# Optimization experiments

Measured on AMD Instinct MI355X. Metric: run time of the kernel, lower is better.

Reference implementation:

```python
import jax, jax.numpy as jnp
import numpy as np

B, P, H, W = 8, 128, 32, 32
NC = 4                 # num_classes = NUM_REL_GROUP + 1
DOBJ = 4424            # 2*DOBJ = 8848
CIN = 256
C = 128 + 8848         # 8976 GCN channel dim


def setup_inputs() -> dict:
    key = jax.random.key(0)
    ks = jax.random.split(key, 24)
    s = 0.02  # weight scale to keep activations moderate
    inp = {
        "x": jax.random.normal(ks[0], (B, CIN, H, W), jnp.float32),
        "rel_pair_idxs": jax.random.randint(ks[1], (B, P, 2), 0, 640, dtype=jnp.int32),
        "obj_rep": jax.random.normal(ks[2], (640, DOBJ), jnp.float32),
        # ADD_GCN params
        "fc_w": jax.random.normal(ks[3], (NC, CIN), jnp.float32) * s,
        "ct_w": jax.random.normal(ks[4], (128, CIN), jnp.float32) * s,
        "ct_b": jnp.zeros((128,), jnp.float32),
        # DynamicGraphConvolution params
        "A": jax.random.normal(ks[5], (NC, NC), jnp.float32) * 0.25,          # static_adj conv1d (no bias)
        "sw_w": jax.random.normal(ks[6], (C, C), jnp.float32) * s / np.sqrt(C) * 30,
        "sw_b": jnp.zeros((C,), jnp.float32),
        "cg_w": jax.random.normal(ks[7], (C, C), jnp.float32) * s / np.sqrt(C) * 30,
        "cg_b": jnp.zeros((C,), jnp.float32),
        "bn_g": jnp.ones((C,), jnp.float32),
        "bn_b": jnp.zeros((C,), jnp.float32),
        "bn_m": jnp.zeros((C,), jnp.float32),
        "bn_v": jnp.ones((C,), jnp.float32),
        "co_w": jax.random.normal(ks[8], (NC, 2 * C), jnp.float32) * s / np.sqrt(C) * 30,
        "co_b": jnp.zeros((NC,), jnp.float32),
        "dw_w": jax.random.normal(ks[9], (C, C), jnp.float32) * s / np.sqrt(C) * 30,
        "dw_b": jnp.zeros((C,), jnp.float32),
        "ll_w": jax.random.normal(ks[10], (NC, C), jnp.float32) * s / np.sqrt(C) * 30,
        "ll_b": jnp.zeros((NC,), jnp.float32),
        "mask_mat": jnp.eye(NC, dtype=jnp.float32),
    }
    return inp


def reference(x, rel_pair_idxs, obj_rep, fc_w, ct_w, ct_b, A, sw_w, sw_b,
              cg_w, cg_b, bn_g, bn_b, bn_m, bn_v, co_w, co_b, dw_w, dw_b,
              ll_w, ll_b, mask_mat):
    leaky = lambda t: jax.nn.leaky_relu(t, 0.2)
    b, cin, h, w = x.shape
    xr = x.reshape(b, cin, h * w)                                  # (B,256,HW)

    # forward_classification_sm: fc -> topk(1).mean == max over spatial
    y = jnp.einsum('oc,bcs->bos', fc_w, xr)                        # (B,NC,HW)
    out1 = y.max(-1)                                               # (B,NC)

    # forward_sam
    mask = jax.nn.sigmoid(y)                                       # (B,NC,HW)
    v = jnp.einsum('oc,bcs->bos', ct_w, xr) + ct_b[None, :, None]  # (B,128,HW)
    v = jnp.einsum('bcs,bns->bcn', v, mask)                        # (B,128,NC)

    # pairwise object features (gather), tiled over NC node slots
    o1 = obj_rep[rel_pair_idxs[..., 0]]                            # (B,P,DOBJ)
    o2 = obj_rep[rel_pair_idxs[..., 1]]
    pf = jnp.concatenate([o1, o2], -1)                             # (B,P,8848)
    p = pf.shape[1]
    pf = jnp.broadcast_to(pf[..., None], pf.shape + (NC,))         # (B,P,8848,NC)
    vb = jnp.broadcast_to(v[:, None], (b, p) + v.shape[1:])        # (B,P,128,NC)
    g = jnp.concatenate([pf, vb], 2).reshape(b * p, C, NC)         # (BP,C,NC)

    # --- DynamicGraphConvolution ---
    # static GCN: node-mix conv1d (no bias) + leaky, then channel 1x1 conv + leaky
    xs = leaky(jnp.einsum('nm,pcm->pcn', A, g))                    # (BP,C,NC)
    xs = leaky(jnp.einsum('oc,pcn->pon', sw_w, xs) + sw_b[None, :, None])
    hg = g + xs

    # dynamic adjacency
    glb = hg.mean(-1)                                              # (BP,C) gap
    glb = glb @ cg_w.T + cg_b                                      # conv_global (1x1)
    glb = (glb - bn_m) * jax.lax.rsqrt(bn_v + 1e-5) * bn_g + bn_b  # BN (eval)
    glb = leaky(glb)
    # conv_create_co_mat over cat([glb_expand, hg], ch) without materializing cat
    adj = jax.nn.sigmoid(
        jnp.einsum('oc,pc->po', co_w[:, :C], glb)[:, :, None]
        + jnp.einsum('oc,pcn->pon', co_w[:, C:], hg)
        + co_b[None, :, None])                                     # (BP,NC,NC)

    # dynamic GCN
    hd = leaky(jnp.einsum('pcn,pnm->pcm', hg, adj))
    z = leaky(jnp.einsum('oc,pcn->pon', dw_w, hd) + dw_b[None, :, None])  # (BP,C,NC)

    # head: last_linear + leaky, masked diagonal sum
    out2 = leaky(jnp.einsum('oc,pcn->pon', ll_w, z) + ll_b[None, :, None])  # (BP,NC,NC)
    out2 = (out2 * jax.lax.stop_gradient(mask_mat)).sum(-1)        # (BP,NC)

    o1b = jnp.broadcast_to(out1[:, None], (b, p, NC)).reshape(b * p, NC)
    return ((o1b + out2) * 0.5).reshape(b, p, NC)
```

## Files before the change

kernel.cpp:

```cpp
#include <hip/hip_runtime.h>
#include <stdint.h>

#define DEVI __device__ __forceinline__

typedef unsigned short u16;
typedef __bf16 bf16x8 __attribute__((ext_vector_type(8)));
typedef float f32x4 __attribute__((ext_vector_type(4)));
typedef u16 u16x8 __attribute__((ext_vector_type(8)));

DEVI u16 f2bf(float f){
  union { float f; unsigned u; } v; v.f = f;
  unsigned r = v.u + 0x7FFFu + ((v.u >> 16) & 1u);
  return (u16)(r >> 16);
}
DEVI float bf2f(u16 h){
  union { unsigned u; float f; } v; v.u = ((unsigned)h) << 16;
  return v.f;
}
DEVI float lky(float t){ return t > 0.f ? t : 0.2f * t; }

#define GLD16(gp, lp) __builtin_amdgcn_global_load_lds( \
    (const __attribute__((address_space(1))) void*)(gp), \
    (__attribute__((address_space(3))) void*)(lp), 16, 0, 0)

template<int EPI>
__global__ __launch_bounds__(1024, 4)
void gemmU(const u16* __restrict__ A, const u16* __restrict__ B,
           int Kp, int Nt, int SN, int Mreal, float* __restrict__ C, long long ldc,
           const float* __restrict__ bias, const float* __restrict__ scale,
           const float* __restrict__ off, const float* __restrict__ llw,
           float* __restrict__ oacc)
{
  __shared__ __align__(16) u16 As[2][16384];
  __shared__ __align__(16) u16 Bs[2][16384];
  const int t    = threadIdx.x;
  const int lane = t & 63;
  const int wid  = t >> 6;
  const int wr = wid >> 2, wc = wid & 3;
  const int l4 = lane >> 4, l15 = lane & 15;

  const int nwg = gridDim.x;
  const int xc = blockIdx.x & 7, pp = blockIdx.x >> 3;
  const int qq = nwg >> 3, rr = nwg & 7;
  const int wg = (xc < rr ? xc*(qq+1) : rr*(qq+1) + (xc-rr)*qq) + pp;
  const int strip_sz = (nwg / Nt) * SN;
  const int strip = wg / strip_sz, srem = wg % strip_sz;
  const int mt = srem / SN, nt = strip*SN + srem % SN;

  const size_t am0 = (size_t)mt*256;
  const size_t bn0 = (size_t)nt*256;

  f32x4 acc[4][4];
  #pragma unroll
  for (int i = 0; i < 4; ++i)
    #pragma unroll
    for (int j = 0; j < 4; ++j) acc[i][j] = f32x4{0.f,0.f,0.f,0.f};
  bf16x8 afr[4], bfr[4];

  const int NT = Kp >> 6;

  const int srl0 = t >> 3, ssl = t & 7;
  const u16* pA = A + (am0 + srl0)*(size_t)Kp;
  const u16* pB = B + (bn0 + srl0)*(size_t)Kp;
  const size_t rowskip = (size_t)128 * Kp;
  const int sco0 = ((ssl ^ (srl0 & 7))*8);
  const int sco1 = ((ssl ^ ((srl0+128) & 7))*8);

  int aoff[4], boff[4];
  #pragma unroll
  for (int mi = 0; mi < 4; ++mi){
    const int r = wr*64 + mi*16 + l15;
    aoff[mi] = r*64 + ((r & 7)*8);
  }
  #pragma unroll
  for (int ni = 0; ni < 4; ++ni){
    const int r = wc*64 + ni*16 + l15;
    boff[ni] = r*64 + ((r & 7)*8);
  }

  auto STAGE = [&](int kc, int buf){
    u16* la = &As[buf][0]; u16* lb = &Bs[buf][0];
    GLD16(pA + kc + sco0,           la + t*8);
    GLD16(pA + rowskip + kc + sco1, la + 8192 + t*8);
    GLD16(pB + kc + sco0,           lb + t*8);
    GLD16(pB + rowskip + kc + sco1, lb + 8192 + t*8);
  };

  STAGE(0, 0);
  asm volatile("s_waitcnt vmcnt(0)" ::: "memory");
  __builtin_amdgcn_s_barrier();

  #define GU_BODY(KT, RB_, WB_)                                              \
  {                                                                          \
    const int nx = ((KT)+1 < NT) ? (KT)+1 : NT-1;                            \
    STAGE(nx*64, WB_);                                                       \
    const u16* ab = &As[RB_][0];                                             \
    const u16* bb = &Bs[RB_][0];                                             \
    _Pragma("unroll")                                                        \
    for (int ks = 0; ks < 2; ++ks){                                          \
      const int sx = (ks*4 + l4)*8;                                          \
      _Pragma("unroll")                                                      \
      for (int mi = 0; mi < 4; ++mi)                                         \
        afr[mi] = *(const bf16x8*)&ab[aoff[mi] ^ sx];                        \
      _Pragma("unroll")                                                      \
      for (int ni = 0; ni < 4; ++ni)                                         \
        bfr[ni] = *(const bf16x8*)&bb[boff[ni] ^ sx];                        \
      __builtin_amdgcn_s_setprio(1);                                         \
      _Pragma("unroll")                                                      \
      for (int mi = 0; mi < 4; ++mi)                                         \
        _Pragma("unroll")                                                    \
        for (int ni = 0; ni < 4; ++ni)                                       \
          acc[mi][ni] = __builtin_amdgcn_mfma_f32_16x16x32_bf16(             \
              afr[mi], bfr[ni], acc[mi][ni], 0, 0, 0);                       \
      __builtin_amdgcn_s_setprio(0);                                         \
    }                                                                        \
    asm volatile("s_waitcnt vmcnt(0)" ::: "memory");                         \
    __builtin_amdgcn_s_barrier();                                            \
  }

  for (int kt = 0; kt < NT; kt += 2){
    GU_BODY(kt,   0, 1);
    GU_BODY(kt+1, 1, 0);
  }
  #undef GU_BODY

  const int ob0 = mt*256 + wr*64;
  const int nb0 = nt*256 + wc*64;

  if (EPI == 0){
    #pragma unroll
    for (int mi = 0; mi < 4; ++mi){
      const int ob = ob0 + mi*16 + l4*4;
      if (ob < Mreal){
        #pragma unroll
        for (int ni = 0; ni < 4; ++ni){
          const int n = nb0 + ni*16 + l15;
          *(f32x4*)&C[(size_t)n*ldc + ob] = acc[mi][ni];
        }
      }
    }
  } else if (EPI == 2){
    #pragma unroll
    for (int ni = 0; ni < 4; ++ni){
      const int n = nb0 + ni*16 + l15;
      float sa0=0.f, sa1=0.f, sa2=0.f, sa3=0.f;
      #pragma unroll
      for (int mi = 0; mi < 4; ++mi){
        const int ob = ob0 + mi*16 + l4*4;
        if (ob < Mreal){
          const float sc0=scale[ob],sc1=scale[ob+1],sc2=scale[ob+2],sc3=scale[ob+3];
          const float of0=off[ob],of1=off[ob+1],of2=off[ob+2],of3=off[ob+3];
          f32x4 a = acc[mi][ni];
          f32x4 vv = { lky(a[0]*sc0+of0), lky(a[1]*sc1+of1),
                       lky(a[2]*sc2+of2), lky(a[3]*sc3+of3) };
          *(f32x4*)&C[(size_t)n*ldc + ob] = vv;
          #pragma unroll
          for (int r = 0; r < 4; ++r){
            const float vr = vv[r];
            sa0 += llw[(size_t)0*17952 + ob + r] * vr;
            sa1 += llw[(size_t)1*17952 + ob + r] * vr;
            sa2 += llw[(size_t)2*17952 + ob + r] * vr;
            sa3 += llw[(size_t)3*17952 + ob + r] * vr;
          }
        }
      }
      float sv[4] = {sa0,sa1,sa2,sa3};
      #pragma unroll
      for (int a4 = 0; a4 < 4; ++a4){
        float tt = sv[a4];
        tt += __shfl_xor(tt, 16);
        tt += __shfl_xor(tt, 32);
        if (l4 == 0) atomicAdd(&oacc[n*4 + a4], tt);
      }
    }
  } else {
    #pragma unroll
    for (int ni = 0; ni < 4; ++ni){
      const int n = nb0 + ni*16 + l15;
      const int m = n & 3, q = n >> 2;
      float s = 0.f;
      #pragma unroll
      for (int mi = 0; mi < 4; ++mi){
        #pragma unroll
        for (int r = 0; r < 4; ++r){
          const int o = ob0 + mi*16 + l4*4 + r;
          if (o < Mreal){
            const float val = lky(acc[mi][ni][r] + bias[o]);
            s += llw[(size_t)m*8976 + o] * val;
          }
        }
      }
      s += __shfl_xor(s, 16);
      s += __shfl_xor(s, 32);
      if (l4 == 0) atomicAdd(&oacc[(q*4 + m)*4 + m], s);
    }
  }
}

__global__ __launch_bounds__(256)
void gemm_vpre(const u16* __restrict__ A, const u16* __restrict__ B,
               int Kp, int Nt, int Mreal, float* __restrict__ C, long long ldc,
               const float* __restrict__ bias)
{
  __shared__ __align__(16) u16 As[2][4096];
  __shared__ __align__(16) u16 Bs[2][4096];
  const int tid  = threadIdx.x;
  const int lane = tid & 63;
  const int wr   = (tid >> 6) >> 1, wc = (tid >> 6) & 1;
  const int l4   = lane >> 4, l15 = lane & 15;
  const int mt   = blockIdx.x / Nt, nt = blockIdx.x % Nt;

  const size_t arow = (size_t)(mt*128 + (tid>>2)) * Kp + (tid&3)*8;
  const size_t brow = (size_t)(nt*128 + (tid>>2)) * Kp + (tid&3)*8;
  const int    ldst = (tid>>2)*32 + (tid&3)*8;
  const size_t rowskip = (size_t)64 * Kp;

  f32x4 acc[4][4];
  #pragma unroll
  for (int i=0;i<4;i++)
    #pragma unroll
    for (int j=0;j<4;j++) acc[i][j] = f32x4{0.f,0.f,0.f,0.f};

  const int NT = Kp >> 5;
  {
    const u16* a0 = A + arow; const u16* b0 = B + brow;
    GLD16(a0,           &As[0][ldst]);
    GLD16(a0 + rowskip, &As[0][ldst + 2048]);
    GLD16(b0,           &Bs[0][ldst]);
    GLD16(b0 + rowskip, &Bs[0][ldst + 2048]);
  }
  __syncthreads();

  for (int kt=0; kt<NT; ++kt){
    const int cur = kt & 1;
    if (kt + 1 < NT){
      const u16* a0 = A + arow + (size_t)(kt+1)*32;
      const u16* b0 = B + brow + (size_t)(kt+1)*32;
      GLD16(a0,           &As[cur^1][ldst]);
      GLD16(a0 + rowskip, &As[cur^1][ldst + 2048]);
      GLD16(b0,           &Bs[cur^1][ldst]);
      GLD16(b0 + rowskip, &Bs[cur^1][ldst + 2048]);
    }
    bf16x8 af[4], bf[4];
    #pragma unroll
    for (int mi=0;mi<4;mi++)
      af[mi] = *(const bf16x8*)&As[cur][(wr*64 + mi*16 + l15)*32 + l4*8];
    #pragma unroll
    for (int ni=0;ni<4;ni++)
      bf[ni] = *(const bf16x8*)&Bs[cur][(wc*64 + ni*16 + l15)*32 + l4*8];
    #pragma unroll
    for (int mi=0;mi<4;mi++)
      #pragma unroll
      for (int ni=0;ni<4;ni++)
        acc[mi][ni] = __builtin_amdgcn_mfma_f32_16x16x32_bf16(af[mi], bf[ni], acc[mi][ni], 0, 0, 0);
    __syncthreads();
  }

  const int ob0 = mt*128 + wr*64;
  const int nb0 = nt*128 + wc*64;
  #pragma unroll
  for (int mi=0;mi<4;mi++)
    #pragma unroll
    for (int r=0;r<4;r++){
      const int o = ob0 + mi*16 + l4*4 + r;
      if (o < Mreal){
        const float bb = bias[o];
        #pragma unroll
        for (int ni=0;ni<4;ni++){
          const int n = nb0 + ni*16 + l15;
          C[(size_t)o*ldc + n] = acc[mi][ni][r] + bb;
        }
      }
    }
}

__global__ void k_cvt_pad(const float* __restrict__ src, int srows, int scols,
                          int lds_, int koff, u16* __restrict__ dst, int Kp)
{
  const int r = blockIdx.x;
  const int nch = Kp >> 3;
  for (int ch = threadIdx.x; ch < nch; ch += blockDim.x){
    const int k = ch*8;
    u16 o[8];
    if (r < srows){
      #pragma unroll
      for (int i=0;i<8;i++){
        const int kk = k + i;
        o[i] = (kk < scols) ? f2bf(src[(size_t)r*lds_ + koff + kk]) : (u16)0;
      }
    } else {
      #pragma unroll
      for (int i=0;i<8;i++) o[i] = 0;
    }
    u16x8 vv = { o[0],o[1],o[2],o[3],o[4],o[5],o[6],o[7] };
    *(u16x8*)&dst[(size_t)r*Kp + k] = vv;
  }
}

__global__ void k_cvt_sww(const float* __restrict__ src, u16* __restrict__ dst)
{
  const int r = blockIdx.x;
  const float* row = src + (size_t)r*8976;
  u16* d1 = dst + (size_t)r*4480;
  u16* d2 = dst + (size_t)(8976+r)*4480;
  for (int ch = threadIdx.x; ch < 560; ch += 256){
    const int k = ch*8;
    u16 a[8], b[8];
    #pragma unroll
    for (int i=0;i<8;i++){
      const int kk = k+i;
      a[i] = (kk < 4424) ? f2bf(row[kk])        : (u16)0;
      b[i] = (kk < 4424) ? f2bf(row[4424 + kk]) : (u16)0;
    }
    u16x8 va = { a[0],a[1],a[2],a[3],a[4],a[5],a[6],a[7] };
    u16x8 vb = { b[0],b[1],b[2],b[3],b[4],b[5],b[6],b[7] };
    *(u16x8*)&d1[k] = va;
    *(u16x8*)&d2[k] = vb;
  }
}

__global__ void k_cvt_obj(const float* __restrict__ obj, u16* __restrict__ dst)
{
  const int r = blockIdx.x;
  const int ab = (r >= 640);
  const float* src = obj + (size_t)(ab ? r-640 : r)*4424;
  for (int ch = threadIdx.x; ch < 560; ch += 256){
    const int k = ch*8;
    u16 o[8];
    #pragma unroll
    for (int i=0;i<8;i++){
      const int kk = k+i;
      float f = (kk < 4424) ? src[kk] : 0.f;
      if (ab) f = fabsf(f);
      o[i] = f2bf(f);
    }
    u16x8 vv = { o[0],o[1],o[2],o[3],o[4],o[5],o[6],o[7] };
    *(u16x8*)&dst[(size_t)r*4480 + k] = vv;
  }
}

__global__ void k_xT(const float* __restrict__ x, u16* __restrict__ xT)
{
  __shared__ float t[32][33];
  const int bid = blockIdx.x;
  const int b = bid >> 8; const int cs = (bid >> 5) & 7; const int ss = bid & 31;
  const int tx = threadIdx.x & 31, ty = threadIdx.x >> 5;
  #pragma unroll
  for (int i=0;i<4;i++){
    const int r = ty + i*8;
    t[r][tx] = x[((size_t)(b*256 + cs*32 + r))*1024 + ss*32 + tx];
  }
  __syncthreads();
  #pragma unroll
  for (int i=0;i<4;i++){
    const int r = ty + i*8;
    xT[((size_t)(b*1024 + ss*32 + r))*256 + cs*32 + tx] = f2bf(t[tx][r]);
  }
}

__global__ void k_ymask(const float* __restrict__ x, const float* __restrict__ fcw,
                        float* __restrict__ y, float* __restrict__ mask)
{
  __shared__ float fc[1024];
  const int b = blockIdx.x >> 2, st = blockIdx.x & 3;
  for (int i=threadIdx.x; i<1024; i+=256) fc[i] = fcw[i];
  __syncthreads();
  const int s = st*256 + threadIdx.x;
  float a0=0,a1=0,a2=0,a3=0;
  for (int c=0;c<256;c++){
    const float xv = x[((size_t)(b*256+c))*1024 + s];
    a0 += fc[c]*xv; a1 += fc[256+c]*xv; a2 += fc[512+c]*xv; a3 += fc[768+c]*xv;
  }
  const size_t base = (size_t)(b*4)*1024 + s;
  y[base]        = a0; mask[base]        = 1.f/(1.f+expf(-a0));
  y[base+1024]   = a1; mask[base+1024]   = 1.f/(1.f+expf(-a1));
  y[base+2048]   = a2; mask[base+2048]   = 1.f/(1.f+expf(-a2));
  y[base+3072]   = a3; mask[base+3072]   = 1.f/(1.f+expf(-a3));
}

__global__ void k_out1(const float* __restrict__ y, float* __restrict__ out1){
  const int bn = blockIdx.x;
  float m = -3.4e38f;
  for (int s=threadIdx.x; s<1024; s+=256) m = fmaxf(m, y[(size_t)bn*1024+s]);
  for (int o=32;o;o>>=1) m = fmaxf(m, __shfl_xor(m,o));
  __shared__ float red[4];
  if ((threadIdx.x&63)==0) red[threadIdx.x>>6] = m;
  __syncthreads();
  if (threadIdx.x==0) out1[bn] = fmaxf(fmaxf(red[0],red[1]),fmaxf(red[2],red[3]));
}

__global__ void k_v(const float* __restrict__ vpreT, const float* __restrict__ mask,
                    float* __restrict__ v){
  const int b = blockIdx.x >> 7, j = blockIdx.x & 127;
  float a[4]={0,0,0,0};
  for (int s=threadIdx.x; s<1024; s+=256){
    const float pv = vpreT[(size_t)j*8192 + b*1024 + s];
    #pragma unroll
    for (int m=0;m<4;m++) a[m] += pv * mask[((size_t)(b*4+m))*1024 + s];
  }
  __shared__ float red[4][5];
  #pragma unroll
  for (int m=0;m<4;m++){
    float t=a[m];
    for (int o=32;o;o>>=1) t += __shfl_xor(t,o);
    if ((threadIdx.x&63)==0) red[m][threadIdx.x>>6]=t;
  }
  __syncthreads();
  if (threadIdx.x<4)
    v[(size_t)(b*128+j)*4 + threadIdx.x] =
      red[threadIdx.x][0]+red[threadIdx.x][1]+red[threadIdx.x][2]+red[threadIdx.x][3];
}

__global__ void k_lv(const float* __restrict__ Am, const float* __restrict__ v,
                     float* __restrict__ lv){
  const int idx = blockIdx.x*256 + threadIdx.x;
  if (idx < 1024){
    #pragma unroll
    for (int n=0;n<4;n++){
      float s=0;
      #pragma unroll
      for (int m=0;m<4;m++) s += Am[n*4+m]*v[idx*4+m];
      lv[idx*4+n] = lky(s);
    }
  }
}

__global__ void k_sV(const float* __restrict__ sw, const float* __restrict__ lv,
                     float* __restrict__ sV){
  __shared__ float l[4096];
  for (int i=threadIdx.x; i<4096; i+=256) l[i]=lv[i];
  __syncthreads();
  const int o = blockIdx.x*256 + threadIdx.x;
  if (o >= 8976) return;
  float acc[8][4] = {};
  const float* row = sw + (size_t)o*8976 + 8848;
  for (int j=0;j<128;j++){
    const float wv = row[j];
    #pragma unroll
    for (int b=0;b<8;b++){
      const float* lb = &l[(b*128+j)*4];
      #pragma unroll
      for (int n=0;n<4;n++) acc[b][n] += wv*lb[n];
    }
  }
  #pragma unroll
  for (int b=0;b<8;b++){
    f32x4 vv = {acc[b][0],acc[b][1],acc[b][2],acc[b][3]};
    *(f32x4*)&sV[((size_t)b*8976 + o)*4] = vv;
  }
}

__global__ void k_so(const float* __restrict__ cgb, const float* __restrict__ g,
                     const float* __restrict__ b2, const float* __restrict__ m,
                     const float* __restrict__ vvar, float* __restrict__ so){
  const int o = blockIdx.x*256+threadIdx.x;
  if (o<8976){
    const float sc = g[o]*rsqrtf(vvar[o]+1e-5f);
    so[o]=sc; so[8976+o] = (cgb[o]-m[o])*sc + b2[o];
  }
}

__global__ void k_glb_t2(const float* __restrict__ U, const float* __restrict__ obj,
                         const int* __restrict__ rel,
                         const float* __restrict__ sV, const float* __restrict__ swb,
                         const float* __restrict__ v, const float* __restrict__ Am,
                         const float* __restrict__ cow, u16* __restrict__ glbB,
                         float* __restrict__ t2)
{
  const int q = blockIdx.x; const int b = q >> 7;
  const int i1 = rel[q*2], i2 = rel[q*2+1];
  const float* u1  = U + (size_t)i1*17952;
  const float* u2  = U + (size_t)i2*17952 + 8976;
  const float* u1a = U + (size_t)(640+i1)*17952;
  const float* u2a = U + (size_t)(640+i2)*17952 + 8976;
  const float* o1 = obj + (size_t)i1*4424;
  const float* o2 = obj + (size_t)i2*4424;
  float rA[4], aA[4];
  #pragma unroll
  for (int n=0;n<4;n++){
    const float s = Am[n*4]+Am[n*4+1]+Am[n*4+2]+Am[n*4+3];
    rA[n]=0.6f*s; aA[n]=0.4f*fabsf(s);
  }
  float t2a[16] = {};
  for (int c = threadIdx.x; c < 9088; c += 256){
    if (c < 8976){
      const float p1 = u1[c] + u2[c];
      const float p2 = u1a[c] + u2a[c];
      const f32x4 sv = *(const f32x4*)&sV[((size_t)b*8976 + c)*4];
      const float sb = swb[c];
      const float gs = (c < 4424) ? o1[c] : (c < 8848) ? o2[c-4424] : 0.f;
      float hg[4]; float sum = 0.f;
      #pragma unroll
      for (int n=0;n<4;n++){
        const float xs2 = lky(rA[n]*p1 + aA[n]*p2 + sv[n] + sb);
        const float g = (c < 8848) ? gs : v[((size_t)b*128 + (c-8848))*4 + n];
        hg[n] = g + xs2; sum += hg[n];
      }
      glbB[(size_t)q*9088 + c] = f2bf(0.25f*sum);
      #pragma unroll
      for (int o4=0;o4<4;o4++){
        const float cw = cow[(size_t)o4*17952 + 8976 + c];
        #pragma unroll
        for (int n=0;n<4;n++) t2a[o4*4+n] += cw*hg[n];
      }
    } else {
      glbB[(size_t)q*9088 + c] = 0;
    }
  }
  __shared__ float red[16][5];
  #pragma unroll
  for (int i=0;i<16;i++){
    float t = t2a[i];
    for (int o=32;o;o>>=1) t += __shfl_xor(t,o);
    if ((threadIdx.x&63)==0) red[i][threadIdx.x>>6]=t;
  }
  __syncthreads();
  if (threadIdx.x < 16)
    t2[q*16+threadIdx.x] = red[threadIdx.x][0]+red[threadIdx.x][1]
                          +red[threadIdx.x][2]+red[threadIdx.x][3];
}

__global__ void k_hd(const float* __restrict__ U, const float* __restrict__ obj,
                     const int* __restrict__ rel,
                     const float* __restrict__ sV, const float* __restrict__ swb,
                     const float* __restrict__ v, const float* __restrict__ Am,
                     const float* __restrict__ co1acc, const float* __restrict__ t2,
                     const float* __restrict__ cob, u16* __restrict__ hdb)
{
  const int q = blockIdx.x; const int b = q>>7;
  const int i1 = rel[q*2], i2 = rel[q*2+1];
  const float* u1  = U + (size_t)i1*17952;
  const float* u2  = U + (size_t)i2*17952 + 8976;
  const float* u1a = U + (size_t)(640+i1)*17952;
  const float* u2a = U + (size_t)(640+i2)*17952 + 8976;
  const float* o1 = obj + (size_t)i1*4424;
  const float* o2 = obj + (size_t)i2*4424;
  float rA[4], aA[4];
  #pragma unroll
  for (int n=0;n<4;n++){
    const float s = Am[n*4]+Am[n*4+1]+Am[n*4+2]+Am[n*4+3];
    rA[n]=0.6f*s; aA[n]=0.4f*fabsf(s);
  }
  __shared__ float aj[16];
  if (threadIdx.x<16){
    const int a_=threadIdx.x>>2, m=threadIdx.x&3;
    const float tt = co1acc[q*4+a_] + t2[q*16 + a_*4 + m] + cob[a_];
    aj[threadIdx.x] = 1.f/(1.f+expf(-tt));
  }
  __syncthreads();
  float ajr[16];
  #pragma unroll
  for (int i=0;i<16;i++) ajr[i]=aj[i];
  for (int c=threadIdx.x; c<9088; c+=256){
    if (c<8976){
      const float p1 = u1[c] + u2[c];
      const float p2 = u1a[c] + u2a[c];
      const f32x4 sv = *(const f32x4*)&sV[((size_t)b*8976 + c)*4];
      const float sb = swb[c];
      const float gs = (c < 4424) ? o1[c] : (c < 8848) ? o2[c-4424] : 0.f;
      float hg[4];
      #pragma unroll
      for (int n=0;n<4;n++){
        const float xs2 = lky(rA[n]*p1 + aA[n]*p2 + sv[n] + sb);
        const float g = (c < 8848) ? gs : v[((size_t)b*128 + (c-8848))*4 + n];
        hg[n] = g + xs2;
      }
      #pragma unroll
      for (int m=0;m<4;m++){
        const float hv = lky(hg[0]*ajr[m] + hg[1]*ajr[4+m] + hg[2]*ajr[8+m] + hg[3]*ajr[12+m]);
        hdb[((size_t)(q*4+m))*9088 + c] = f2bf(hv);
      }
    } else {
      #pragma unroll
      for (int m=0;m<4;m++) hdb[((size_t)(q*4+m))*9088 + c] = 0;
    }
  }
}

__global__ void k_final(const float* __restrict__ o2f, const float* __restrict__ out1,
                        const float* __restrict__ llb, const float* __restrict__ mm,
                        float* __restrict__ out)
{
  const int idx = blockIdx.x*256+threadIdx.x;
  if (idx < 4096){
    const int q = idx>>2, o = idx&3, b = q>>7;
    float s=0.f;
    #pragma unroll
    for (int m=0;m<4;m++) s += lky(o2f[(q*4+o)*4+m] + llb[o]) * mm[o*4+m];
    out[idx] = 0.5f*(out1[b*4+o] + s);
  }
}

extern "C" void kernel_launch(void* const* d_in, const int* in_sizes, int n_in,
                              void* d_out, int out_size, void* d_ws, size_t ws_size,
                              hipStream_t stream)
{
  const float* x    = (const float*)d_in[0];
  const int*   rel  = (const int*)d_in[1];
  const float* obj  = (const float*)d_in[2];
  const float* fcw  = (const float*)d_in[3];
  const float* ctw  = (const float*)d_in[4];
  const float* ctb  = (const float*)d_in[5];
  const float* Am   = (const float*)d_in[6];
  const float* sww  = (const float*)d_in[7];
  const float* swb  = (const float*)d_in[8];
  const float* cgw  = (const float*)d_in[9];
  const float* cgb  = (const float*)d_in[10];
  const float* bng  = (const float*)d_in[11];
  const float* bnb  = (const float*)d_in[12];
  const float* bnm  = (const float*)d_in[13];
  const float* bnv  = (const float*)d_in[14];
  const float* cow  = (const float*)d_in[15];
  const float* cob  = (const float*)d_in[16];
  const float* dww  = (const float*)d_in[17];
  const float* dwb  = (const float*)d_in[18];
  const float* llw  = (const float*)d_in[19];
  const float* llb  = (const float*)d_in[20];
  const float* mm   = (const float*)d_in[21];
  float* out = (float*)d_out;
  (void)in_sizes; (void)n_in; (void)out_size; (void)ws_size;

  char* ws = (char*)d_ws;
  size_t off = 0;
  auto alloc = [&](size_t bytes)->char*{
    char* p = ws + off; off = (off + bytes + 255) & ~(size_t)255; return p;
  };
  u16*   Wb    = (u16*)  alloc((size_t)9216*9088*2);
  float* U     = (float*)alloc((size_t)1280*17952*4);
  u16*   glbB  = (u16*)  alloc((size_t)1024*9088*2);
  u16*   hdb   = (u16*)  alloc((size_t)4096*9088*2);
  u16*   objB  = (u16*)  alloc((size_t)1280*4480*2);
  float* glb2  = (float*)alloc((size_t)1024*8976*4);
  u16*   xT    = (u16*)  alloc((size_t)8192*256*2);
  u16*   ctwb  = (u16*)  alloc((size_t)128*256*2);
  float* y     = (float*)alloc((size_t)32768*4);
  float* mask  = (float*)alloc((size_t)32768*4);
  float* out1  = (float*)alloc((size_t)32*4);
  float* vpreT = (float*)alloc((size_t)128*8192*4);
  float* v     = (float*)alloc((size_t)4096*4);
  float* lv    = (float*)alloc((size_t)4096*4);
  float* sV    = (float*)alloc((size_t)287232*4);
  float* so    = (float*)alloc((size_t)2*8976*4);
  float* t2    = (float*)alloc((size_t)16384*4);
  float* co1a  = (float*)alloc((size_t)4096*4);
  float* o2f   = (float*)alloc((size_t)16384*4);

  k_xT<<<dim3(2048), dim3(256), 0, stream>>>(x, xT);
  k_cvt_pad<<<dim3(128), dim3(256), 0, stream>>>(ctw, 128, 256, 256, 0, ctwb, 256);
  k_ymask<<<dim3(32), dim3(256), 0, stream>>>(x, fcw, y, mask);
  k_out1<<<dim3(32), dim3(256), 0, stream>>>(y, out1);
  gemm_vpre<<<dim3(64), dim3(256), 0, stream>>>(
      ctwb, xT, 256, 64, 128, vpreT, (long long)8192, ctb);
  k_v<<<dim3(1024), dim3(256), 0, stream>>>(vpreT, mask, v);

  k_cvt_obj<<<dim3(1280), dim3(256), 0, stream>>>(obj, objB);
  k_cvt_sww<<<dim3(8976), dim3(256), 0, stream>>>(sww, Wb);
  gemmU<0><<<dim3(71*5), dim3(1024), 0, stream>>>(
      Wb, objB, 4480, 5, 5, 17952, U, (long long)17952,
      nullptr, nullptr, nullptr, nullptr, nullptr);

  k_lv<<<dim3(4), dim3(256), 0, stream>>>(Am, v, lv);
  k_sV<<<dim3(36), dim3(256), 0, stream>>>(sww, lv, sV);
  k_glb_t2<<<dim3(1024), dim3(256), 0, stream>>>(U, obj, rel, sV, swb, v, Am,
                                                 cow, glbB, t2);

  k_cvt_pad<<<dim3(9216), dim3(256), 0, stream>>>(cgw, 8976, 8976, 8976, 0, Wb, 9088);
  k_so<<<dim3(36), dim3(256), 0, stream>>>(cgb, bng, bnb, bnm, bnv, so);
  hipMemsetAsync(co1a, 0, (size_t)4096*4, stream);
  gemmU<2><<<dim3(36*4), dim3(1024), 0, stream>>>(
      Wb, glbB, 9088, 4, 4, 8976, glb2, (long long)8976,
      nullptr, so, so + 8976, cow, co1a);

  k_cvt_pad<<<dim3(9216), dim3(256), 0, stream>>>(dww, 8976, 8976, 8976, 0, Wb, 9088);
  k_hd<<<dim3(1024), dim3(256), 0, stream>>>(U, obj, rel, sV, swb, v, Am,
                                             co1a, t2, cob, hdb);

  hipMemsetAsync(o2f, 0, (size_t)16384*4, stream);
  gemmU<3><<<dim3(36*16), dim3(1024), 0, stream>>>(
      Wb, hdb, 9088, 16, 8, 8976, nullptr, 0, dwb,
      nullptr, nullptr, llw, o2f);

  k_final<<<dim3(16), dim3(256), 0, stream>>>(o2f, out1, llb, mm, out);
}
```

Measured before the change: 1.992 ms.

## Fuse fp32-to-bf16 weight conversion into GEMM A-operand loads

Drops the separate weight conversion kernels (k_cvt_sww and two k_cvt_pad calls) and their bf16 workspace buffer. The GEMM now reads fp32 weights straight from global memory into registers, converts them to bf16 and writes them into swizzled LDS, with bounds masking and a stacked-row mapping for the split sw_w case. This removes a full write and re-read of large bf16 weight matrices per call. In exchange, A-operand traffic per tile doubles (fp32) and is re-read by every N-tile, and the async global-to-LDS path for A becomes register staging with conversion ALU work.

```diff
diff --git a/kernel.cpp b/kernel.cpp
--- a/kernel.cpp
+++ b/kernel.cpp
@@ -23,9 +23,10 @@
     (const __attribute__((address_space(1))) void*)(gp), \
     (__attribute__((address_space(3))) void*)(lp), 16, 0, 0)
 
-template<int EPI>
+template<int EPI, int STACKED>
 __global__ __launch_bounds__(1024, 4)
-void gemmU(const u16* __restrict__ A, const u16* __restrict__ B,
+void gemmV(const float* __restrict__ A, int Astride, int Kreal, int Mrows,
+           const u16* __restrict__ B,
            int Kp, int Nt, int SN, int Mreal, float* __restrict__ C, long long ldc,
            const float* __restrict__ bias, const float* __restrict__ scale,
            const float* __restrict__ off, const float* __restrict__ llw,
@@ -47,7 +48,7 @@
   const int strip = wg / strip_sz, srem = wg % strip_sz;
   const int mt = srem / SN, nt = strip*SN + srem % SN;
 
-  const size_t am0 = (size_t)mt*256;
+  const int am0 = mt*256;
   const size_t bn0 = (size_t)nt*256;
 
   f32x4 acc[4][4];
@@ -59,12 +60,45 @@
 
   const int NT = Kp >> 6;
 
-  const int srl0 = t >> 3, ssl = t & 7;
-  const u16* pA = A + (am0 + srl0)*(size_t)Kp;
-  const u16* pB = B + (bn0 + srl0)*(size_t)Kp;
-  const size_t rowskip = (size_t)128 * Kp;
-  const int sco0 = ((ssl ^ (srl0 & 7))*8);
-  const int sco1 = ((ssl ^ ((srl0+128) & 7))*8);
+  const int trl = t >> 3, tsl = t & 7;
+  const int scol = ((tsl ^ (trl & 7)) * 8);
+  const u16* pB0 = B + (bn0 + trl)*(size_t)Kp + scol;
+  const u16* pB1 = B + (bn0 + trl + 128)*(size_t)Kp + scol;
+
+  const int row0 = am0 + trl;
+  const int row1 = row0 + 128;
+  int ro0 = row0, ko0 = 0, ro1 = row1, ko1 = 0;
+  if (STACKED){
+    if (row0 >= 8976){ ro0 = row0 - 8976; ko0 = 4424; }
+    if (row1 >= 8976){ ro1 = row1 - 8976; ko1 = 4424; }
+  }
+  const bool okr0 = row0 < Mrows, okr1 = row1 < Mrows;
+  const float* pA0 = A + (size_t)(okr0 ? ro0 : 0)*Astride + (okr0 ? ko0 : 0) + scol;
+  const float* pA1 = A + (size_t)(okr1 ? ro1 : 0)*Astride + (okr1 ? ko1 : 0) + scol;
+
+  f32x4 ra0a, ra0b, ra1a, ra1b;
+  auto ALOAD = [&](int kc){
+    const bool okc = (kc + scol) < Kreal;
+    const f32x4 z = {0.f,0.f,0.f,0.f};
+    const bool ok0 = okr0 && okc, ok1 = okr1 && okc;
+    ra0a = ok0 ? *(const f32x4*)(pA0 + kc)     : z;
+    ra0b = ok0 ? *(const f32x4*)(pA0 + kc + 4) : z;
+    ra1a = ok1 ? *(const f32x4*)(pA1 + kc)     : z;
+    ra1b = ok1 ? *(const f32x4*)(pA1 + kc + 4) : z;
+  };
+  auto AWRITE = [&](int buf){
+    u16x8 w0 = { f2bf(ra0a[0]),f2bf(ra0a[1]),f2bf(ra0a[2]),f2bf(ra0a[3]),
+                 f2bf(ra0b[0]),f2bf(ra0b[1]),f2bf(ra0b[2]),f2bf(ra0b[3]) };
+    u16x8 w1 = { f2bf(ra1a[0]),f2bf(ra1a[1]),f2bf(ra1a[2]),f2bf(ra1a[3]),
+                 f2bf(ra1b[0]),f2bf(ra1b[1]),f2bf(ra1b[2]),f2bf(ra1b[3]) };
+    *(u16x8*)&As[buf][t*8] = w0;
+    *(u16x8*)&As[buf][8192 + t*8] = w1;
+  };
+  auto BSTAGE = [&](int kc, int buf){
+    u16* lb = &Bs[buf][0];
+    GLD16(pB0 + kc, lb + t*8);
+    GLD16(pB1 + kc, lb + 8192 + t*8);
+  };
 
   int aoff[4], boff[4];
   #pragma unroll
@@ -78,22 +112,17 @@
     boff[ni] = r*64 + ((r & 7)*8);
   }
 
-  auto STAGE = [&](int kc, int buf){
-    u16* la = &As[buf][0]; u16* lb = &Bs[buf][0];
-    GLD16(pA + kc + sco0,           la + t*8);
-    GLD16(pA + rowskip + kc + sco1, la + 8192 + t*8);
-    GLD16(pB + kc + sco0,           lb + t*8);
-    GLD16(pB + rowskip + kc + sco1, lb + 8192 + t*8);
-  };
-
-  STAGE(0, 0);
-  asm volatile("s_waitcnt vmcnt(0)" ::: "memory");
+  ALOAD(0);
+  BSTAGE(0, 0);
+  AWRITE(0);
+  asm volatile("s_waitcnt vmcnt(0) lgkmcnt(0)" ::: "memory");
   __builtin_amdgcn_s_barrier();
 
-  #define GU_BODY(KT, RB_, WB_)                                              \
+  #define GV_BODY(KT, RB_, WB_)                                              \
   {                                                                          \
     const int nx = ((KT)+1 < NT) ? (KT)+1 : NT-1;                            \
-    STAGE(nx*64, WB_);                                                       \
+    ALOAD(nx*64);                                                            \
+    BSTAGE(nx*64, WB_);                                                      \
     const u16* ab = &As[RB_][0];                                             \
     const u16* bb = &Bs[RB_][0];                                             \
     _Pragma("unroll")                                                        \
@@ -114,15 +143,16 @@
               afr[mi], bfr[ni], acc[mi][ni], 0, 0, 0);                       \
       __builtin_amdgcn_s_setprio(0);                                         \
     }                                                                        \
-    asm volatile("s_waitcnt vmcnt(0)" ::: "memory");                         \
+    AWRITE(WB_);                                                             \
+    asm volatile("s_waitcnt vmcnt(0) lgkmcnt(0)" ::: "memory");              \
     __builtin_amdgcn_s_barrier();                                            \
   }
 
   for (int kt = 0; kt < NT; kt += 2){
-    GU_BODY(kt,   0, 1);
-    GU_BODY(kt+1, 1, 0);
-  }
-  #undef GU_BODY
+    GV_BODY(kt,   0, 1);
+    GV_BODY(kt+1, 1, 0);
+  }
+  #undef GV_BODY
 
   const int ob0 = mt*256 + wr*64;
   const int nb0 = nt*256 + wc*64;
@@ -294,28 +324,6 @@
     }
     u16x8 vv = { o[0],o[1],o[2],o[3],o[4],o[5],o[6],o[7] };
     *(u16x8*)&dst[(size_t)r*Kp + k] = vv;
-  }
-}
-
-__global__ void k_cvt_sww(const float* __restrict__ src, u16* __restrict__ dst)
-{
-  const int r = blockIdx.x;
-  const float* row = src + (size_t)r*8976;
-  u16* d1 = dst + (size_t)r*4480;
-  u16* d2 = dst + (size_t)(8976+r)*4480;
-  for (int ch = threadIdx.x; ch < 560; ch += 256){
-    const int k = ch*8;
-    u16 a[8], b[8];
-    #pragma unroll
-    for (int i=0;i<8;i++){
-      const int kk = k+i;
-      a[i] = (kk < 4424) ? f2bf(row[kk])        : (u16)0;
-      b[i] = (kk < 4424) ? f2bf(row[4424 + kk]) : (u16)0;
-    }
-    u16x8 va = { a[0],a[1],a[2],a[3],a[4],a[5],a[6],a[7] };
-    u16x8 vb = { b[0],b[1],b[2],b[3],b[4],b[5],b[6],b[7] };
-    *(u16x8*)&d1[k] = va;
-    *(u16x8*)&d2[k] = vb;
   }
 }
 
@@ -625,7 +633,6 @@
   auto alloc = [&](size_t bytes)->char*{
     char* p = ws + off; off = (off + bytes + 255) & ~(size_t)255; return p;
   };
-  u16*   Wb    = (u16*)  alloc((size_t)9216*9088*2);
   float* U     = (float*)alloc((size_t)1280*17952*4);
   u16*   glbB  = (u16*)  alloc((size_t)1024*9088*2);
   u16*   hdb   = (u16*)  alloc((size_t)4096*9088*2);
@@ -654,9 +661,8 @@
   k_v<<<dim3(1024), dim3(256), 0, stream>>>(vpreT, mask, v);
 
   k_cvt_obj<<<dim3(1280), dim3(256), 0, stream>>>(obj, objB);
-  k_cvt_sww<<<dim3(8976), dim3(256), 0, stream>>>(sww, Wb);
-  gemmU<0><<<dim3(71*5), dim3(1024), 0, stream>>>(
-      Wb, objB, 4480, 5, 5, 17952, U, (long long)17952,
+  gemmV<0,1><<<dim3(71*5), dim3(1024), 0, stream>>>(
+      sww, 8976, 4424, 17952, objB, 4480, 5, 5, 17952, U, (long long)17952,
       nullptr, nullptr, nullptr, nullptr, nullptr);
 
   k_lv<<<dim3(4), dim3(256), 0, stream>>>(Am, v, lv);
@@ -664,21 +670,19 @@
   k_glb_t2<<<dim3(1024), dim3(256), 0, stream>>>(U, obj, rel, sV, swb, v, Am,
                                                  cow, glbB, t2);
 
-  k_cvt_pad<<<dim3(9216), dim3(256), 0, stream>>>(cgw, 8976, 8976, 8976, 0, Wb, 9088);
   k_so<<<dim3(36), dim3(256), 0, stream>>>(cgb, bng, bnb, bnm, bnv, so);
   hipMemsetAsync(co1a, 0, (size_t)4096*4, stream);
-  gemmU<2><<<dim3(36*4), dim3(1024), 0, stream>>>(
-      Wb, glbB, 9088, 4, 4, 8976, glb2, (long long)8976,
+  gemmV<2,0><<<dim3(36*4), dim3(1024), 0, stream>>>(
+      cgw, 8976, 8976, 8976, glbB, 9088, 4, 4, 8976, glb2, (long long)8976,
       nullptr, so, so + 8976, cow, co1a);
 
-  k_cvt_pad<<<dim3(9216), dim3(256), 0, stream>>>(dww, 8976, 8976, 8976, 0, Wb, 9088);
   k_hd<<<dim3(1024), dim3(256), 0, stream>>>(U, obj, rel, sV, swb, v, Am,
                                              co1a, t2, cob, hdb);
 
   hipMemsetAsync(o2f, 0, (size_t)16384*4, stream);
-  gemmU<3><<<dim3(36*16), dim3(1024), 0, stream>>>(
-      Wb, hdb, 9088, 16, 8, 8976, nullptr, 0, dwb,
-      nullptr, nullptr, llw, o2f);
+  gemmV<3,0><<<dim3(36*16), dim3(1024), 0, stream>>>(
+      dww, 8976, 8976, 8976, hdb, 9088, 16, 8, 8976, nullptr, 0,
+      dwb, nullptr, nullptr, llw, o2f);
 
   k_final<<<dim3(16), dim3(256), 0, stream>>>(o2f, out1, llb, mm, out);
 }
```

After: 5.280 ms. 2.65x slower.
